# Optimization experiments

Measured on AMD Instinct MI355X. Metric: run time of the kernel, lower is better.

Reference implementation:

```python
import jax, jax.numpy as jnp
import numpy as np

NUM_NODES = 100000
N = 65536          # subgraph nodes returned by LastNeighborLoader
E = 655360         # N * size(=10) last-neighbor edges
B = 4096           # temporal event batch
MEM = 128          # memory_dim (== pos_embedding_dim)
TIME = 64          # time_dim
MSG = 64           # raw_msg_dim
EMB = 128          # embedding_dim (gnn out_channels)
HEADS = 2
HD = EMB // HEADS  # 64, TransformerConv out_channels//2 per head
HID = 64           # mlp_hidden_dim[-1]
IN = 2 * MEM       # gnn in_channels (memory || pos memory)
EDGE_D = MSG + TIME


def setup_inputs() -> dict:
    key = jax.random.key(0)
    ks = jax.random.split(key, 32)
    nrm = lambda i, shp, s=1.0: jax.random.normal(ks[i], shp, jnp.float32) * s
    inp = {}
    # data / state tensors
    inp["memory"] = nrm(0, (NUM_NODES, MEM))
    inp["pos_memory"] = nrm(1, (NUM_NODES, MEM))
    inp["last_update"] = jax.random.uniform(ks[2], (NUM_NODES,), jnp.float32) * 1000.0
    inp["n_id"] = jnp.arange(N, dtype=jnp.int32)
    inp["edge_index"] = jax.random.randint(ks[3], (2, E), 0, N, dtype=jnp.int32)
    inp["edge_t"] = jax.random.uniform(ks[4], (E,), jnp.float32) * 1000.0
    inp["edge_msg"] = nrm(5, (E, MSG))
    inp["src"] = jax.random.randint(ks[6], (B,), 0, N, dtype=jnp.int32)
    inp["dst"] = jax.random.randint(ks[7], (B,), 0, N, dtype=jnp.int32)
    inp["neg_dst"] = jax.random.randint(ks[8], (B,), 0, N, dtype=jnp.int32)
    # learned parameters
    inp["time_w"] = nrm(9, (1, TIME))                      # TimeEncoder Linear(1, time_dim)
    inp["time_b"] = nrm(10, (TIME,), 0.1)
    sI = 1.0 / np.sqrt(IN); sE = 1.0 / np.sqrt(EDGE_D)
    inp["Wq"] = nrm(11, (IN, HEADS * HD), sI); inp["bq"] = jnp.zeros((HEADS * HD,), jnp.float32)
    inp["Wk"] = nrm(12, (IN, HEADS * HD), sI); inp["bk"] = jnp.zeros((HEADS * HD,), jnp.float32)
    inp["Wv"] = nrm(13, (IN, HEADS * HD), sI); inp["bv"] = jnp.zeros((HEADS * HD,), jnp.float32)
    inp["We"] = nrm(14, (EDGE_D, HEADS * HD), sE); inp["be"] = jnp.zeros((HEADS * HD,), jnp.float32)
    inp["Wskip"] = nrm(15, (IN, EMB), sI); inp["bskip"] = jnp.zeros((EMB,), jnp.float32)
    inp["mlp_w"] = nrm(16, (EMB, HID), 1.0 / np.sqrt(EMB)); inp["mlp_b"] = jnp.zeros((HID,), jnp.float32)
    sH = 1.0 / np.sqrt(HID)
    inp["lps_w"] = nrm(17, (HID, HID), sH); inp["lps_b"] = jnp.zeros((HID,), jnp.float32)
    inp["lpd_w"] = nrm(18, (HID, HID), sH); inp["lpd_b"] = jnp.zeros((HID,), jnp.float32)
    inp["lpf_w"] = nrm(19, (HID, 1), sH); inp["lpf_b"] = jnp.zeros((1,), jnp.float32)
    return inp


def reference(memory, pos_memory, last_update, n_id, edge_index, edge_t, edge_msg,
              src, dst, neg_dst, time_w, time_b, Wq, bq, Wk, bk, Wv, bv, We, be,
              Wskip, bskip, mlp_w, mlp_b, lps_w, lps_b, lpd_w, lpd_b, lpf_w, lpf_b):
    Nn = n_id.shape[0]
    # assoc remap: global node id -> local row in subgraph
    assoc = jnp.zeros((NUM_NODES,), jnp.int32).at[n_id].set(jnp.arange(Nn, dtype=jnp.int32))
    # memory read + positional memory concat  -> [N, 2*MEM]
    z = jnp.concatenate([memory[n_id], pos_memory[n_id]], axis=-1)
    lu = last_update[n_id]                                # [N]
    se, de = edge_index[0], edge_index[1]                 # source (j), target (i)
    # time encoding of relative time: cos(Linear(1->TIME))
    rel_t = lu[se] - edge_t                               # [E]
    t_enc = jnp.cos(rel_t[:, None] * time_w[0][None, :] + time_b)  # [E, TIME]
    edge_attr = jnp.concatenate([t_enc, edge_msg], axis=-1)        # [E, TIME+MSG]
    # TransformerConv (heads=2, concat): q from target, k/v from source (+edge)
    q = (z @ Wq + bq).reshape(Nn, HEADS, HD)
    k = (z @ Wk + bk).reshape(Nn, HEADS, HD)
    v = (z @ Wv + bv).reshape(Nn, HEADS, HD)
    e = (edge_attr @ We + be).reshape(-1, HEADS, HD)
    ke = k[se] + e                                        # [E, H, HD]
    ve = v[se] + e
    score = jnp.sum(q[de] * ke, axis=-1) / jnp.sqrt(jnp.float32(HD))  # [E, H]
    # segment softmax over incoming edges of each target node
    smax = jax.ops.segment_max(score, de, num_segments=Nn)
    ex = jnp.exp(score - smax[de])
    denom = jax.ops.segment_sum(ex, de, num_segments=Nn)
    alpha = ex / (denom[de] + 1e-16)                      # [E, H]
    agg = jax.ops.segment_sum(alpha[..., None] * ve, de, num_segments=Nn)  # [N, H, HD]
    out = agg.reshape(Nn, HEADS * HD) + (z @ Wskip + bskip)  # root/skip connection
    # MLP([embedding_dim, hidden]) -> single Linear (last layer: no act/norm)
    h = out @ mlp_w + mlp_b                               # [N, HID]
    z_src = h[assoc[src]]; z_dst = h[assoc[dst]]; z_neg = h[assoc[neg_dst]]
    def link_pred(a, b):
        hh = jax.nn.relu(a @ lps_w + lps_b + b @ lpd_w + lpd_b)
        return hh @ lpf_w + lpf_b
    pos_out = link_pred(z_src, z_dst)                     # [B, 1]
    neg_out = link_pred(z_src, z_neg)                     # [B, 1]
    return pos_out, neg_out
```

## Files before the change

kernel.cpp:

```cpp
#include <hip/hip_runtime.h>
#include <math.h>

#define NNODES 100000
#define NSUB   65536
#define NEDGE  655360
#define NBATCH 4096
#define LDK 72

typedef __attribute__((ext_vector_type(8))) short short8;
typedef __attribute__((ext_vector_type(4))) float f32x4;

__device__ __forceinline__ unsigned short f2bf(float x) {
  unsigned int b = __float_as_uint(x);
  b += 0x7fffu + ((b >> 16) & 1u);
  return (unsigned short)(b >> 16);
}
__device__ __forceinline__ float bf2f(unsigned short u) {
  return __uint_as_float(((unsigned int)u) << 16);
}
__device__ __forceinline__ float bflo(unsigned int u) { return __uint_as_float(u << 16); }
__device__ __forceinline__ float bfhi(unsigned int u) { return __uint_as_float(u & 0xffff0000u); }
__device__ __forceinline__ unsigned int pk2(float a, float b) {
  return (unsigned int)f2bf(a) | ((unsigned int)f2bf(b) << 16);
}
__device__ __forceinline__ void unpack8(uint4 u, float* a, float* b) {
  a[0] = bflo(u.x); b[0] = bfhi(u.x);
  a[1] = bflo(u.y); b[1] = bfhi(u.y);
  a[2] = bflo(u.z); b[2] = bfhi(u.z);
  a[3] = bflo(u.w); b[3] = bfhi(u.w);
}
__device__ __forceinline__ ushort4 pkv4(float a, float b, float c, float d) {
  return make_ushort4(f2bf(a), f2bf(b), f2bf(c), f2bf(d));
}

__global__ void k_sentinel(float* out) { out[0] = -12345.0f; }

__global__ void k_packW(const float* __restrict__ Wq, const float* __restrict__ bq,
                        const float* __restrict__ Wk, const float* __restrict__ bk,
                        const float* __restrict__ Wv, const float* __restrict__ bv,
                        const float* __restrict__ Ws, const float* __restrict__ bs,
                        const float* __restrict__ We,
                        unsigned short* __restrict__ Wt, float* __restrict__ bias) {
  int n = blockIdx.x, r = threadIdx.x;
  float v = 0.f, bn = 0.f;
  if (n < 128) {
    int l = n >> 1, h = n & 1;
    v = Wq[r * 128 + h * 64 + l] * 0.125f; bn = bq[h * 64 + l] * 0.125f;
  } else if (n < 256) {
    int i = n - 128, l = i >> 1, h = i & 1;
    v = Wk[r * 128 + h * 64 + l]; bn = bk[h * 64 + l];
  } else if (n < 384) {
    int i = n - 256, l = i >> 1, h = i & 1;
    v = Wv[r * 128 + h * 64 + l]; bn = bv[h * 64 + l];
  } else if (n < 512) {
    int c = n - 384; v = Ws[r * 128 + c]; bn = bs[c];
  } else {
    int i = (n < 640) ? (n - 512) : (n - 640);
    int c = i >> 1, h = i & 1;
    int kk = (n < 640) ? c : (64 + c);
    float s = 0.f;
    for (int d = 0; d < 64; d++) s += Wq[r * 128 + h * 64 + d] * We[kk * 128 + h * 64 + d];
    v = s * 0.125f;
    if (r == 0) {
      float sb = 0.f;
      for (int d = 0; d < 64; d++) sb += bq[h * 64 + d] * We[kk * 128 + h * 64 + d];
      bn = sb * 0.125f;
    }
  }
  Wt[(size_t)n * 256 + r] = f2bf(v);
  if (r == 0) bias[n] = bn;
}

__global__ void k_packW2(const float* __restrict__ We, const float* __restrict__ mlp_w,
                         unsigned short* __restrict__ W2t) {
  int r = blockIdx.x, j = threadIdx.x;
  float v;
  if (r < 128) v = mlp_w[r * 64 + j];
  else if (r < 192) { int k = r - 128; float s = 0; for (int c = 0; c < 64; c++) s += We[k * 128 + c] * mlp_w[c * 64 + j]; v = s; }
  else if (r < 256) { int k = r - 192; float s = 0; for (int c = 0; c < 64; c++) s += We[(64 + k) * 128 + c] * mlp_w[c * 64 + j]; v = s; }
  else if (r < 320) { int k = r - 256; float s = 0; for (int c = 0; c < 64; c++) s += We[k * 128 + 64 + c] * mlp_w[(64 + c) * 64 + j]; v = s; }
  else if (r < 384) { int k = r - 320; float s = 0; for (int c = 0; c < 64; c++) s += We[(64 + k) * 128 + 64 + c] * mlp_w[(64 + c) * 64 + j]; v = s; }
  else v = mlp_w[(r - 384) * 64 + j];
  W2t[(size_t)j * 512 + r] = f2bf(v);
}

__global__ void k_bem(const float* __restrict__ be, const float* __restrict__ mlp_w,
                      float* __restrict__ bem) {
  int h = blockIdx.x, j = threadIdx.x;
  float s = 0.f;
  for (int c = 0; c < 64; c++) s += be[h * 64 + c] * mlp_w[(h * 64 + c) * 64 + j];
  bem[h * 64 + j] = s;
}

__global__ void k_assoc(const int* __restrict__ n_id, int* __restrict__ assoc) {
  int i = blockIdx.x * 256 + threadIdx.x;
  if (i < NSUB) assoc[n_id[i]] = i;
}

__global__ void k_packA(const float* __restrict__ mem, const float* __restrict__ pmem,
                        const int* __restrict__ n_id, unsigned short* __restrict__ anodes) {
  int i = blockIdx.x * 256 + threadIdx.x;
  int node = i >> 5, ch = i & 31;
  int nid = n_id[node];
  const float* src = (ch < 16) ? (mem + (size_t)nid * 128 + ch * 8)
                               : (pmem + (size_t)nid * 128 + (ch - 16) * 8);
  float4 f0 = *(const float4*)src, f1 = *(const float4*)(src + 4);
  uint4 o;
  o.x = pk2(f0.x, f0.y); o.y = pk2(f0.z, f0.w);
  o.z = pk2(f1.x, f1.y); o.w = pk2(f1.z, f1.w);
  *(uint4*)(anodes + (size_t)node * 256 + ch * 8) = o;
}

__global__ void k_prep_edge(const int* __restrict__ edge_index, const int* __restrict__ n_id,
                            const float* __restrict__ last_update, const float* __restrict__ edge_t,
                            float* __restrict__ rel_t, int* __restrict__ deg) {
  int e = blockIdx.x * 256 + threadIdx.x;
  if (e < NEDGE) {
    rel_t[e] = last_update[n_id[edge_index[e]]] - edge_t[e];
    atomicAdd(&deg[edge_index[NEDGE + e]], 1);
  }
}

__global__ __launch_bounds__(1024)
void k_scan(const int* __restrict__ deg, int* __restrict__ offs, int* __restrict__ cursor) {
  __shared__ int wsum[16];
  __shared__ int carry_s;
  int t = threadIdx.x, w = t >> 6, l = t & 63;
  if (t == 0) carry_s = 0;
  __syncthreads();
  for (int base = 0; base < NSUB; base += 1024) {
    int i = base + t;
    int v = deg[i];
    int s = v;
    #pragma unroll
    for (int d = 1; d < 64; d <<= 1) {
      int u = __shfl_up(s, d, 64);
      if (l >= d) s += u;
    }
    if (l == 63) wsum[w] = s;
    __syncthreads();
    int woff = 0;
    for (int k2 = 0; k2 < w; k2++) woff += wsum[k2];
    int total = 0;
    for (int k2 = 0; k2 < 16; k2++) total += wsum[k2];
    int c = carry_s;
    int excl = c + woff + s - v;
    offs[i] = excl; cursor[i] = excl;
    __syncthreads();
    if (t == 0) carry_s = c + total;
    __syncthreads();
  }
  if (t == 0) { offs[NSUB] = carry_s; cursor[NSUB] = carry_s; }
}

__global__ void k_scatter(const int* __restrict__ edge_index, int* __restrict__ cursor,
                          int* __restrict__ csr) {
  int e = blockIdx.x * 256 + threadIdx.x;
  if (e < NEDGE) {
    int p = atomicAdd(&cursor[edge_index[NEDGE + e]], 1);
    csr[p] = e;
  }
}

__global__ __launch_bounds__(256)
void k_gemm_node(const unsigned short* __restrict__ anodes, const unsigned short* __restrict__ Wt,
                 const float* __restrict__ bias, unsigned short* __restrict__ nodeout) {
  __shared__ unsigned short sA[128][LDK];
  __shared__ unsigned short sB[128][LDK];
  int t = threadIdx.x;
  int row0 = blockIdx.x * 128, n0 = blockIdx.y * 128;
  int ar = t >> 1, ak = (t & 1) * 32;
  int w = t >> 6, lane = t & 63, quad = lane >> 4, r16 = lane & 15;
  int m_off = (w >> 1) * 64, n_off = (w & 1) * 64;
  f32x4 acc[4][4] = {};
  for (int st = 0; st < 4; st++) {
    int ks = st * 64;
    __syncthreads();
    #pragma unroll
    for (int i = 0; i < 4; i++)
      *(uint4*)&sA[ar][ak + i * 8] = *(const uint4*)(anodes + (size_t)(row0 + ar) * 256 + ks + ak + i * 8);
    #pragma unroll
    for (int i = 0; i < 4; i++)
      *(uint4*)&sB[ar][ak + i * 8] = *(const uint4*)(Wt + (size_t)(n0 + ar) * 256 + ks + ak + i * 8);
    __syncthreads();
    #pragma unroll
    for (int kk = 0; kk < 2; kk++) {
      short8 af[4], bf_[4];
      #pragma unroll
      for (int i = 0; i < 4; i++) af[i]  = *(const short8*)&sA[m_off + i * 16 + r16][kk * 32 + quad * 8];
      #pragma unroll
      for (int i = 0; i < 4; i++) bf_[i] = *(const short8*)&sB[n_off + i * 16 + r16][kk * 32 + quad * 8];
      #pragma unroll
      for (int i = 0; i < 4; i++)
        #pragma unroll
        for (int j = 0; j < 4; j++)
          acc[i][j] = __builtin_amdgcn_mfma_f32_16x16x32_bf16(af[i], bf_[j], acc[i][j], 0, 0, 0);
    }
  }
  #pragma unroll
  for (int j = 0; j < 4; j++) {
    int col = n0 + n_off + j * 16 + r16;
    float bv_ = bias[col];
    #pragma unroll
    for (int i = 0; i < 4; i++) {
      int rbase = row0 + m_off + i * 16 + quad * 4;
      #pragma unroll
      for (int rg = 0; rg < 4; rg++)
        nodeout[(size_t)(rbase + rg) * 768 + col] = f2bf(acc[i][j][rg] + bv_);
    }
  }
}

__global__ __launch_bounds__(256)
void k_edge(const unsigned short* __restrict__ nodeout, const int* __restrict__ edge_index,
            const float* __restrict__ rel_t, const float* __restrict__ edge_msg,
            const float* __restrict__ time_w, const float* __restrict__ time_b,
            const float* __restrict__ be, const int* __restrict__ offs,
            const int* __restrict__ csr, unsigned short* __restrict__ aggbuf,
            float* __restrict__ salph) {
  int t = threadIdx.x, w = t >> 6, lane = t & 63;
  int j = lane & 15;
  int node = blockIdx.x * 16 + w * 4 + (lane >> 4);
  const unsigned short* nr = nodeout + (size_t)node * 768;
  uint4 q4  = *(const uint4*)(nr + 8 * j);
  uint4 qc4 = *(const uint4*)(nr + 512 + 8 * j);
  uint4 qm4 = *(const uint4*)(nr + 640 + 8 * j);
  float4 tw4 = *(const float4*)(time_w + 4 * j);
  float4 tb4 = *(const float4*)(time_b + 4 * j);
  float4 beA = *(const float4*)(be + 4 * j);
  float4 beB = *(const float4*)(be + 64 + 4 * j);
  float q0[4], q1[4], qc0[4], qc1[4], qm0[4], qm1[4];
  unpack8(q4, q0, q1); unpack8(qc4, qc0, qc1); unpack8(qm4, qm0, qm1);
  float qbe0 = q0[0] * beA.x + q0[1] * beA.y + q0[2] * beA.z + q0[3] * beA.w;
  float qbe1 = q1[0] * beB.x + q1[1] * beB.y + q1[2] * beB.z + q1[3] * beB.w;
  #pragma unroll
  for (int s = 1; s < 16; s <<= 1) { qbe0 += __shfl_xor(qbe0, s, 64); qbe1 += __shfl_xor(qbe1, s, 64); }
  float d0 = 0.f, d1 = 0.f;
  float aV0[4] = {}, aV1[4] = {}, aC0[4] = {}, aC1[4] = {}, aM0[4] = {}, aM1[4] = {};
  int e0 = offs[node], e1 = offs[node + 1];
  for (int idx = e0; idx < e1; idx++) {
    int eid = csr[idx];
    int se = edge_index[eid];
    float rt = rel_t[eid];
    const unsigned short* ns = nodeout + (size_t)se * 768;
    uint4 kv = *(const uint4*)(ns + 128 + 8 * j);
    uint4 vv = *(const uint4*)(ns + 256 + 8 * j);
    float4 mg = *(const float4*)(edge_msg + (size_t)eid * 64 + 4 * j);
    float k0[4], k1[4], v0[4], v1[4];
    unpack8(kv, k0, k1); unpack8(vv, v0, v1);
    float cv[4];
    cv[0] = __cosf(rt * tw4.x + tb4.x);
    cv[1] = __cosf(rt * tw4.y + tb4.y);
    cv[2] = __cosf(rt * tw4.z + tb4.z);
    cv[3] = __cosf(rt * tw4.w + tb4.w);
    float p0 = q0[0] * k0[0] + q0[1] * k0[1] + q0[2] * k0[2] + q0[3] * k0[3]
             + qc0[0] * cv[0] + qc0[1] * cv[1] + qc0[2] * cv[2] + qc0[3] * cv[3]
             + qm0[0] * mg.x + qm0[1] * mg.y + qm0[2] * mg.z + qm0[3] * mg.w;
    float p1 = q1[0] * k1[0] + q1[1] * k1[1] + q1[2] * k1[2] + q1[3] * k1[3]
             + qc1[0] * cv[0] + qc1[1] * cv[1] + qc1[2] * cv[2] + qc1[3] * cv[3]
             + qm1[0] * mg.x + qm1[1] * mg.y + qm1[2] * mg.z + qm1[3] * mg.w;
    #pragma unroll
    for (int s = 1; s < 16; s <<= 1) { p0 += __shfl_xor(p0, s, 64); p1 += __shfl_xor(p1, s, 64); }
    float ex0 = __expf(p0 + qbe0), ex1 = __expf(p1 + qbe1);
    d0 += ex0; d1 += ex1;
    float mgc[4] = {mg.x, mg.y, mg.z, mg.w};
    #pragma unroll
    for (int c = 0; c < 4; c++) {
      aV0[c] += ex0 * v0[c]; aC0[c] += ex0 * cv[c]; aM0[c] += ex0 * mgc[c];
      aV1[c] += ex1 * v1[c]; aC1[c] += ex1 * cv[c]; aM1[c] += ex1 * mgc[c];
    }
  }
  float i0 = 1.f / (d0 + 1e-16f), i1 = 1.f / (d1 + 1e-16f);
  unsigned short* ag = aggbuf + (size_t)node * 512;
  *(ushort4*)(ag + 4 * j)       = pkv4(aV0[0] * i0, aV0[1] * i0, aV0[2] * i0, aV0[3] * i0);
  *(ushort4*)(ag + 64 + 4 * j)  = pkv4(aV1[0] * i1, aV1[1] * i1, aV1[2] * i1, aV1[3] * i1);
  *(ushort4*)(ag + 128 + 4 * j) = pkv4(aC0[0] * i0, aC0[1] * i0, aC0[2] * i0, aC0[3] * i0);
  *(ushort4*)(ag + 192 + 4 * j) = pkv4(aM0[0] * i0, aM0[1] * i0, aM0[2] * i0, aM0[3] * i0);
  *(ushort4*)(ag + 256 + 4 * j) = pkv4(aC1[0] * i1, aC1[1] * i1, aC1[2] * i1, aC1[3] * i1);
  *(ushort4*)(ag + 320 + 4 * j) = pkv4(aM1[0] * i1, aM1[1] * i1, aM1[2] * i1, aM1[3] * i1);
  *(uint4*)(ag + 384 + 8 * j)   = *(const uint4*)(nr + 384 + 8 * j);
  if (j == 0) { salph[node * 2] = d0 * i0; salph[node * 2 + 1] = d1 * i1; }
}

__global__ __launch_bounds__(128)
void k_gemm_final(const unsigned short* __restrict__ aggbuf, const unsigned short* __restrict__ W2t,
                  const float* __restrict__ salph, const float* __restrict__ bem,
                  const float* __restrict__ mlp_b, float* __restrict__ h) {
  __shared__ unsigned short sA[128][LDK];
  __shared__ unsigned short sB[64][LDK];
  int t = threadIdx.x;
  int row0 = blockIdx.x * 128;
  int w = t >> 6, lane = t & 63, quad = lane >> 4, r16 = lane & 15;
  int m_off = w * 64;
  f32x4 acc[4][4] = {};
  for (int st = 0; st < 8; st++) {
    int ks = st * 64;
    __syncthreads();
    #pragma unroll
    for (int c = 0; c < 8; c++)
      *(uint4*)&sA[t][c * 8] = *(const uint4*)(aggbuf + (size_t)(row0 + t) * 512 + ks + c * 8);
    int brr = t >> 1;
    #pragma unroll
    for (int jj = 0; jj < 4; jj++) {
      int c = (t & 1) * 4 + jj;
      *(uint4*)&sB[brr][c * 8] = *(const uint4*)(W2t + (size_t)brr * 512 + ks + c * 8);
    }
    __syncthreads();
    #pragma unroll
    for (int kk = 0; kk < 2; kk++) {
      short8 af[4], bf_[4];
      #pragma unroll
      for (int i = 0; i < 4; i++) af[i]  = *(const short8*)&sA[m_off + i * 16 + r16][kk * 32 + quad * 8];
      #pragma unroll
      for (int i = 0; i < 4; i++) bf_[i] = *(const short8*)&sB[i * 16 + r16][kk * 32 + quad * 8];
      #pragma unroll
      for (int i = 0; i < 4; i++)
        #pragma unroll
        for (int jj = 0; jj < 4; jj++)
          acc[i][jj] = __builtin_amdgcn_mfma_f32_16x16x32_bf16(af[i], bf_[jj], acc[i][jj], 0, 0, 0);
    }
  }
  #pragma unroll
  for (int jj = 0; jj < 4; jj++) {
    int col = jj * 16 + r16;
    float mb = mlp_b[col], b0 = bem[col], b1 = bem[64 + col];
    #pragma unroll
    for (int i = 0; i < 4; i++) {
      int rbase = row0 + m_off + i * 16 + quad * 4;
      #pragma unroll
      for (int rg = 0; rg < 4; rg++) {
        int rr = rbase + rg;
        h[(size_t)rr * 64 + col] = acc[i][jj][rg] + mb + salph[rr * 2] * b0 + salph[rr * 2 + 1] * b1;
      }
    }
  }
}

__global__ __launch_bounds__(256)
void k_linkpred(const float* __restrict__ h, const int* __restrict__ assoc,
                const int* __restrict__ src, const int* __restrict__ dst,
                const int* __restrict__ neg, const float* __restrict__ lps_w,
                const float* __restrict__ lps_b, const float* __restrict__ lpd_w,
                const float* __restrict__ lpd_b, const float* __restrict__ lpf_w,
                const float* __restrict__ lpf_b, float* __restrict__ out) {
  int t = threadIdx.x, w = t >> 6, j = t & 63;
  int b = blockIdx.x * 4 + w;
  const float* hs = h + (size_t)assoc[src[b]] * 64;
  const float* hd = h + (size_t)assoc[dst[b]] * 64;
  const float* hn = h + (size_t)assoc[neg[b]] * 64;
  float vs = lps_b[j], vd = lpd_b[j], vn = lpd_b[j];
  for (int k = 0; k < 64; k++) {
    float ws_ = lps_w[k * 64 + j];
    float wd_ = lpd_w[k * 64 + j];
    vs += hs[k] * ws_;
    vd += hd[k] * wd_;
    vn += hn[k] * wd_;
  }
  float fw = lpf_w[j];
  float hp = fmaxf(vs + vd, 0.f) * fw;
  float hq = fmaxf(vs + vn, 0.f) * fw;
  #pragma unroll
  for (int m = 1; m < 64; m <<= 1) {
    hp += __shfl_xor(hp, m, 64);
    hq += __shfl_xor(hq, m, 64);
  }
  if (j == 0) {
    out[b] = hp + lpf_b[0];
    out[NBATCH + b] = hq + lpf_b[0];
  }
}

extern "C" void kernel_launch(void* const* d_in, const int* in_sizes, int n_in,
                              void* d_out, int out_size, void* d_ws, size_t ws_size,
                              hipStream_t stream) {
  if (n_in < 30) return;
  const float* memory      = (const float*)d_in[0];
  const float* pos_memory  = (const float*)d_in[1];
  const float* last_update = (const float*)d_in[2];
  const int*   n_id        = (const int*)d_in[3];
  const int*   edge_index  = (const int*)d_in[4];
  const float* edge_t      = (const float*)d_in[5];
  const float* edge_msg    = (const float*)d_in[6];
  const int*   src         = (const int*)d_in[7];
  const int*   dst         = (const int*)d_in[8];
  const int*   neg_dst     = (const int*)d_in[9];
  const float* time_w      = (const float*)d_in[10];
  const float* time_b      = (const float*)d_in[11];
  const float* Wq = (const float*)d_in[12]; const float* bq = (const float*)d_in[13];
  const float* Wk = (const float*)d_in[14]; const float* bk = (const float*)d_in[15];
  const float* Wv = (const float*)d_in[16]; const float* bv = (const float*)d_in[17];
  const float* We = (const float*)d_in[18]; const float* be = (const float*)d_in[19];
  const float* Wskip = (const float*)d_in[20]; const float* bskip = (const float*)d_in[21];
  const float* mlp_w = (const float*)d_in[22]; const float* mlp_b = (const float*)d_in[23];
  const float* lps_w = (const float*)d_in[24]; const float* lps_b = (const float*)d_in[25];
  const float* lpd_w = (const float*)d_in[26]; const float* lpd_b = (const float*)d_in[27];
  const float* lpf_w = (const float*)d_in[28]; const float* lpf_b = (const float*)d_in[29];
  float* out = (float*)d_out;

  char* ws = (char*)d_ws;
  size_t off = 0;
  auto alloc = [&](size_t bytes) -> void* {
    void* p = ws + off;
    off += (bytes + 255) & ~(size_t)255;
    return p;
  };
  int*   assoc   = (int*)alloc((size_t)NNODES * 4);
  unsigned short* Wt  = (unsigned short*)alloc((size_t)768 * 256 * 2);
  float* bias    = (float*)alloc(768 * 4);
  unsigned short* W2t = (unsigned short*)alloc((size_t)64 * 512 * 2);
  float* bem     = (float*)alloc(128 * 4);
  float* rel_t   = (float*)alloc((size_t)NEDGE * 4);
  unsigned short* anodes  = (unsigned short*)alloc((size_t)NSUB * 256 * 2);
  unsigned short* nodeout = (unsigned short*)alloc((size_t)NSUB * 768 * 2);
  unsigned short* aggbuf  = (unsigned short*)alloc((size_t)NSUB * 512 * 2);
  float* salph   = (float*)alloc((size_t)NSUB * 2 * 4);
  int*   deg     = (int*)alloc((size_t)NSUB * 4);
  int*   offs    = (int*)alloc((size_t)(NSUB + 1) * 4);
  int*   cursor  = (int*)alloc((size_t)(NSUB + 1) * 4);
  int*   csr     = (int*)alloc((size_t)NEDGE * 4);
  float* hbuf    = (float*)alloc((size_t)NSUB * 64 * 4);

  if (ws_size < off) {
    k_sentinel<<<1, 1, 0, stream>>>(out);
    return;
  }

  (void)hipMemsetAsync(deg, 0, (size_t)NSUB * 4, stream);
  k_packW<<<768, 256, 0, stream>>>(Wq, bq, Wk, bk, Wv, bv, Wskip, bskip, We, Wt, bias);
  k_packW2<<<512, 64, 0, stream>>>(We, mlp_w, W2t);
  k_bem<<<2, 64, 0, stream>>>(be, mlp_w, bem);
  k_assoc<<<NSUB / 256, 256, 0, stream>>>(n_id, assoc);
  k_packA<<<NSUB * 32 / 256, 256, 0, stream>>>(memory, pos_memory, n_id, anodes);
  k_prep_edge<<<NEDGE / 256, 256, 0, stream>>>(edge_index, n_id, last_update, edge_t, rel_t, deg);
  k_scan<<<1, 1024, 0, stream>>>(deg, offs, cursor);
  k_scatter<<<NEDGE / 256, 256, 0, stream>>>(edge_index, cursor, csr);
  k_gemm_node<<<dim3(NSUB / 128, 6), 256, 0, stream>>>(anodes, Wt, bias, nodeout);
  k_edge<<<NSUB / 16, 256, 0, stream>>>(nodeout, edge_index, rel_t, edge_msg, time_w, time_b,
                                        be, offs, csr, aggbuf, salph);
  k_gemm_final<<<NSUB / 128, 128, 0, stream>>>(aggbuf, W2t, salph, bem, mlp_b, hbuf);
  k_linkpred<<<NBATCH / 4, 256, 0, stream>>>(hbuf, assoc, src, dst, neg_dst,
                                             lps_w, lps_b, lpd_w, lpd_b, lpf_w, lpf_b, out);
}
```

Measured before the change: 741.6 us.

## Parallelize CSR scan, pack edge metadata, bf16 messages, batch edge gathers

Replaces the single-block serial prefix scan with a three-kernel block-parallel scan. The scatter now writes source id, relative time and edge id into one 16-byte record per CSR slot, which removes the dependent csr→edge_index→rel_t lookups in the edge kernel. Edge messages are converted to bf16 in a separate pass, and the edge loop loads metadata for 16 edges cooperatively, then issues four neighbour gathers before computing, to raise memory-level parallelism. In exchange it adds extra kernels and a full pass over edge_msg, and reduces message precision to bf16.

Measured after the change: 698.7 us. 5.8% less time.

```diff
diff --git a/kernel.cpp b/kernel.cpp
--- a/kernel.cpp
+++ b/kernel.cpp
@@ -121,44 +121,54 @@
   }
 }
 
+__global__ void k_msgb(const float* __restrict__ edge_msg, unsigned int* __restrict__ msgb) {
+  int i = blockIdx.x * 256 + threadIdx.x;
+  float2 f = *(const float2*)(edge_msg + (size_t)i * 2);
+  msgb[i] = pk2(f.x, f.y);
+}
+
 __global__ __launch_bounds__(1024)
-void k_scan(const int* __restrict__ deg, int* __restrict__ offs, int* __restrict__ cursor) {
+void k_scan1(const int* __restrict__ deg, int* __restrict__ excl, int* __restrict__ btot) {
   __shared__ int wsum[16];
-  __shared__ int carry_s;
   int t = threadIdx.x, w = t >> 6, l = t & 63;
-  if (t == 0) carry_s = 0;
+  int i = blockIdx.x * 1024 + t;
+  int v = deg[i], s = v;
+  #pragma unroll
+  for (int d = 1; d < 64; d <<= 1) { int u = __shfl_up(s, d, 64); if (l >= d) s += u; }
+  if (l == 63) wsum[w] = s;
   __syncthreads();
-  for (int base = 0; base < NSUB; base += 1024) {
-    int i = base + t;
-    int v = deg[i];
-    int s = v;
-    #pragma unroll
-    for (int d = 1; d < 64; d <<= 1) {
-      int u = __shfl_up(s, d, 64);
-      if (l >= d) s += u;
-    }
-    if (l == 63) wsum[w] = s;
-    __syncthreads();
-    int woff = 0;
-    for (int k2 = 0; k2 < w; k2++) woff += wsum[k2];
-    int total = 0;
-    for (int k2 = 0; k2 < 16; k2++) total += wsum[k2];
-    int c = carry_s;
-    int excl = c + woff + s - v;
-    offs[i] = excl; cursor[i] = excl;
-    __syncthreads();
-    if (t == 0) carry_s = c + total;
-    __syncthreads();
-  }
-  if (t == 0) { offs[NSUB] = carry_s; cursor[NSUB] = carry_s; }
-}
-
-__global__ void k_scatter(const int* __restrict__ edge_index, int* __restrict__ cursor,
-                          int* __restrict__ csr) {
+  int woff = 0;
+  #pragma unroll
+  for (int k = 0; k < 16; k++) woff += (k < w) ? wsum[k] : 0;
+  excl[i] = woff + s - v;
+  if (t == 1023) btot[blockIdx.x] = woff + s;
+}
+
+__global__ void k_scan2(const int* __restrict__ btot, int* __restrict__ boff,
+                        int* __restrict__ offs, int* __restrict__ cursor) {
+  int l = threadIdx.x;
+  int v = btot[l], s = v;
+  #pragma unroll
+  for (int d = 1; d < 64; d <<= 1) { int u = __shfl_up(s, d, 64); if (l >= d) s += u; }
+  boff[l] = s - v;
+  if (l == 63) { offs[NSUB] = s; cursor[NSUB] = s; }
+}
+
+__global__ __launch_bounds__(1024)
+void k_scan3(const int* __restrict__ excl, const int* __restrict__ boff,
+             int* __restrict__ offs, int* __restrict__ cursor) {
+  int i = blockIdx.x * 1024 + threadIdx.x;
+  int o = excl[i] + boff[blockIdx.x];
+  offs[i] = o; cursor[i] = o;
+}
+
+__global__ void k_scatter(const int* __restrict__ edge_index, const float* __restrict__ rel_t,
+                          int* __restrict__ cursor, uint4* __restrict__ csrmeta) {
   int e = blockIdx.x * 256 + threadIdx.x;
   if (e < NEDGE) {
-    int p = atomicAdd(&cursor[edge_index[NEDGE + e]], 1);
-    csr[p] = e;
+    int de = edge_index[NEDGE + e];
+    int p = atomicAdd(&cursor[de], 1);
+    csrmeta[p] = make_uint4((unsigned)edge_index[e], __float_as_uint(rel_t[e]), (unsigned)e, 0u);
   }
 }
 
@@ -212,11 +222,10 @@
 }
 
 __global__ __launch_bounds__(256)
-void k_edge(const unsigned short* __restrict__ nodeout, const int* __restrict__ edge_index,
-            const float* __restrict__ rel_t, const float* __restrict__ edge_msg,
+void k_edge(const unsigned short* __restrict__ nodeout, const unsigned short* __restrict__ msgb,
             const float* __restrict__ time_w, const float* __restrict__ time_b,
             const float* __restrict__ be, const int* __restrict__ offs,
-            const int* __restrict__ csr, unsigned short* __restrict__ aggbuf,
+            const uint4* __restrict__ csrmeta, unsigned short* __restrict__ aggbuf,
             float* __restrict__ salph) {
   int t = threadIdx.x, w = t >> 6, lane = t & 63;
   int j = lane & 15;
@@ -238,36 +247,57 @@
   float d0 = 0.f, d1 = 0.f;
   float aV0[4] = {}, aV1[4] = {}, aC0[4] = {}, aC1[4] = {}, aM0[4] = {}, aM1[4] = {};
   int e0 = offs[node], e1 = offs[node + 1];
-  for (int idx = e0; idx < e1; idx++) {
-    int eid = csr[idx];
-    int se = edge_index[eid];
-    float rt = rel_t[eid];
-    const unsigned short* ns = nodeout + (size_t)se * 768;
-    uint4 kv = *(const uint4*)(ns + 128 + 8 * j);
-    uint4 vv = *(const uint4*)(ns + 256 + 8 * j);
-    float4 mg = *(const float4*)(edge_msg + (size_t)eid * 64 + 4 * j);
-    float k0[4], k1[4], v0[4], v1[4];
-    unpack8(kv, k0, k1); unpack8(vv, v0, v1);
-    float cv[4];
-    cv[0] = __cosf(rt * tw4.x + tb4.x);
-    cv[1] = __cosf(rt * tw4.y + tb4.y);
-    cv[2] = __cosf(rt * tw4.z + tb4.z);
-    cv[3] = __cosf(rt * tw4.w + tb4.w);
-    float p0 = q0[0] * k0[0] + q0[1] * k0[1] + q0[2] * k0[2] + q0[3] * k0[3]
-             + qc0[0] * cv[0] + qc0[1] * cv[1] + qc0[2] * cv[2] + qc0[3] * cv[3]
-             + qm0[0] * mg.x + qm0[1] * mg.y + qm0[2] * mg.z + qm0[3] * mg.w;
-    float p1 = q1[0] * k1[0] + q1[1] * k1[1] + q1[2] * k1[2] + q1[3] * k1[3]
-             + qc1[0] * cv[0] + qc1[1] * cv[1] + qc1[2] * cv[2] + qc1[3] * cv[3]
-             + qm1[0] * mg.x + qm1[1] * mg.y + qm1[2] * mg.z + qm1[3] * mg.w;
-    #pragma unroll
-    for (int s = 1; s < 16; s <<= 1) { p0 += __shfl_xor(p0, s, 64); p1 += __shfl_xor(p1, s, 64); }
-    float ex0 = __expf(p0 + qbe0), ex1 = __expf(p1 + qbe1);
-    d0 += ex0; d1 += ex1;
-    float mgc[4] = {mg.x, mg.y, mg.z, mg.w};
-    #pragma unroll
-    for (int c = 0; c < 4; c++) {
-      aV0[c] += ex0 * v0[c]; aC0[c] += ex0 * cv[c]; aM0[c] += ex0 * mgc[c];
-      aV1[c] += ex1 * v1[c]; aC1[c] += ex1 * cv[c]; aM1[c] += ex1 * mgc[c];
+  int deg = e1 - e0;
+  int lb = lane & 48;
+  for (int base = 0; base < deg; base += 16) {
+    int cidx = e0 + base + j;
+    int hi = e1 - 1;
+    cidx = cidx > hi ? hi : cidx;
+    uint4 mt = csrmeta[cidx];
+    int rem = deg - base; rem = rem > 16 ? 16 : rem;
+    for (int c = 0; c < rem; c += 4) {
+      uint4 kvr[4], vvr[4];
+      uint2 mgr[4];
+      float rtv[4];
+      #pragma unroll
+      for (int ii = 0; ii < 4; ii++) {
+        int sl = lb | (c + ii);
+        int se_i = __shfl((int)mt.x, sl, 64);
+        rtv[ii] = __uint_as_float((unsigned)__shfl((int)mt.y, sl, 64));
+        int eid_i = __shfl((int)mt.z, sl, 64);
+        const unsigned short* ns = nodeout + (size_t)se_i * 768;
+        kvr[ii] = *(const uint4*)(ns + 128 + 8 * j);
+        vvr[ii] = *(const uint4*)(ns + 256 + 8 * j);
+        mgr[ii] = *(const uint2*)(msgb + (size_t)eid_i * 64 + 4 * j);
+      }
+      #pragma unroll
+      for (int ii = 0; ii < 4; ii++) {
+        float msk = (c + ii < rem) ? 1.f : 0.f;
+        float k0[4], k1[4], v0[4], v1[4];
+        unpack8(kvr[ii], k0, k1); unpack8(vvr[ii], v0, v1);
+        float mgc[4] = {bflo(mgr[ii].x), bfhi(mgr[ii].x), bflo(mgr[ii].y), bfhi(mgr[ii].y)};
+        float rt = rtv[ii];
+        float cv[4];
+        cv[0] = __cosf(rt * tw4.x + tb4.x);
+        cv[1] = __cosf(rt * tw4.y + tb4.y);
+        cv[2] = __cosf(rt * tw4.z + tb4.z);
+        cv[3] = __cosf(rt * tw4.w + tb4.w);
+        float p0 = q0[0] * k0[0] + q0[1] * k0[1] + q0[2] * k0[2] + q0[3] * k0[3]
+                 + qc0[0] * cv[0] + qc0[1] * cv[1] + qc0[2] * cv[2] + qc0[3] * cv[3]
+                 + qm0[0] * mgc[0] + qm0[1] * mgc[1] + qm0[2] * mgc[2] + qm0[3] * mgc[3];
+        float p1 = q1[0] * k1[0] + q1[1] * k1[1] + q1[2] * k1[2] + q1[3] * k1[3]
+                 + qc1[0] * cv[0] + qc1[1] * cv[1] + qc1[2] * cv[2] + qc1[3] * cv[3]
+                 + qm1[0] * mgc[0] + qm1[1] * mgc[1] + qm1[2] * mgc[2] + qm1[3] * mgc[3];
+        #pragma unroll
+        for (int s = 1; s < 16; s <<= 1) { p0 += __shfl_xor(p0, s, 64); p1 += __shfl_xor(p1, s, 64); }
+        float ex0 = __expf(p0 + qbe0) * msk, ex1 = __expf(p1 + qbe1) * msk;
+        d0 += ex0; d1 += ex1;
+        #pragma unroll
+        for (int cc = 0; cc < 4; cc++) {
+          aV0[cc] += ex0 * v0[cc]; aC0[cc] += ex0 * cv[cc]; aM0[cc] += ex0 * mgc[cc];
+          aV1[cc] += ex1 * v1[cc]; aC1[cc] += ex1 * cv[cc]; aM1[cc] += ex1 * mgc[cc];
+        }
+      }
     }
   }
   float i0 = 1.f / (d0 + 1e-16f), i1 = 1.f / (d1 + 1e-16f);
@@ -417,7 +447,11 @@
   int*   deg     = (int*)alloc((size_t)NSUB * 4);
   int*   offs    = (int*)alloc((size_t)(NSUB + 1) * 4);
   int*   cursor  = (int*)alloc((size_t)(NSUB + 1) * 4);
-  int*   csr     = (int*)alloc((size_t)NEDGE * 4);
+  int*   excl    = (int*)alloc((size_t)NSUB * 4);
+  int*   btot    = (int*)alloc(64 * 4);
+  int*   boff    = (int*)alloc(64 * 4);
+  uint4* csrmeta = (uint4*)alloc((size_t)NEDGE * 16);
+  unsigned int* msgb = (unsigned int*)alloc((size_t)NEDGE * 64 * 2);
   float* hbuf    = (float*)alloc((size_t)NSUB * 64 * 4);
 
   if (ws_size < off) {
@@ -432,11 +466,14 @@
   k_assoc<<<NSUB / 256, 256, 0, stream>>>(n_id, assoc);
   k_packA<<<NSUB * 32 / 256, 256, 0, stream>>>(memory, pos_memory, n_id, anodes);
   k_prep_edge<<<NEDGE / 256, 256, 0, stream>>>(edge_index, n_id, last_update, edge_t, rel_t, deg);
-  k_scan<<<1, 1024, 0, stream>>>(deg, offs, cursor);
-  k_scatter<<<NEDGE / 256, 256, 0, stream>>>(edge_index, cursor, csr);
+  k_msgb<<<NEDGE * 32 / 256, 256, 0, stream>>>(edge_msg, msgb);
+  k_scan1<<<NSUB / 1024, 1024, 0, stream>>>(deg, excl, btot);
+  k_scan2<<<1, 64, 0, stream>>>(btot, boff, offs, cursor);
+  k_scan3<<<NSUB / 1024, 1024, 0, stream>>>(excl, boff, offs, cursor);
+  k_scatter<<<NEDGE / 256, 256, 0, stream>>>(edge_index, rel_t, cursor, csrmeta);
   k_gemm_node<<<dim3(NSUB / 128, 6), 256, 0, stream>>>(anodes, Wt, bias, nodeout);
-  k_edge<<<NSUB / 16, 256, 0, stream>>>(nodeout, edge_index, rel_t, edge_msg, time_w, time_b,
-                                        be, offs, csr, aggbuf, salph);
+  k_edge<<<NSUB / 16, 256, 0, stream>>>(nodeout, (const unsigned short*)msgb, time_w, time_b,
+                                        be, offs, csrmeta, aggbuf, salph);
   k_gemm_final<<<NSUB / 128, 128, 0, stream>>>(aggbuf, W2t, salph, bem, mlp_b, hbuf);
   k_linkpred<<<NBATCH / 4, 256, 0, stream>>>(hbuf, assoc, src, dst, neg_dst,
                                              lps_w, lps_b, lpd_w, lpd_b, lpf_w, lpf_b, out);
```
